# Kernel tuning notes

Measured on AMD Instinct MI355X. Metric: run time of the kernel, lower is better.

Reference implementation:

```python
import jax, jax.numpy as jnp
import numpy as np

N_NODES = 50000
N_EDGES = 800000
F_NODE = 64
F_EDGE = 32
F_GLOBAL = 32
OUT_DIM = 64
N_GRAPHS = 256


def setup_inputs() -> dict:
    key = jax.random.key(0)
    ks = jax.random.split(key, 8)
    x = jax.random.normal(ks[0], (N_NODES, F_NODE), dtype=jnp.float32)
    edge_index = jax.random.randint(ks[1], (2, N_EDGES), 0, N_NODES, dtype=jnp.int64)
    edge_attr = jax.random.normal(ks[2], (N_EDGES, F_EDGE), dtype=jnp.float32)
    u = jax.random.normal(ks[3], (N_GRAPHS, F_GLOBAL), dtype=jnp.float32)
    batch = jnp.sort(jax.random.randint(ks[4], (N_NODES,), 0, N_GRAPHS, dtype=jnp.int64))
    # params (scaled like default Linear init)
    W1 = jax.random.normal(ks[5], (F_NODE + F_EDGE, OUT_DIM), dtype=jnp.float32) / np.sqrt(F_NODE + F_EDGE)
    b1 = jnp.zeros((OUT_DIM,), dtype=jnp.float32)
    W2 = jax.random.normal(ks[6], (F_NODE + OUT_DIM + F_GLOBAL, OUT_DIM), dtype=jnp.float32) / np.sqrt(F_NODE + OUT_DIM + F_GLOBAL)
    b2 = jnp.zeros((OUT_DIM,), dtype=jnp.float32)
    return {"x": x, "edge_index": edge_index, "edge_attr": edge_attr,
            "u": u, "batch": batch, "W1": W1, "b1": b1, "W2": W2, "b2": b2}


def reference(x, edge_index, edge_attr, u, batch, W1, b1, W2, b2):
    dest, src = edge_index[0], edge_index[1]
    # gather source node features + edge attrs -> [E, F_NODE + F_EDGE]
    edge_info = jnp.concatenate([x[src], edge_attr], axis=1)
    # node_mlp_1: Linear + ReLU
    edge_messages = jax.nn.relu(edge_info @ W1 + b1)  # [E, OUT_DIM]
    # scatter-sum into destination nodes
    aggregated = jax.ops.segment_sum(edge_messages, dest, num_segments=x.shape[0])  # [N, OUT_DIM]
    # concat node, aggregated messages, per-graph global
    node_info = jnp.concatenate([x, aggregated, u[batch]], axis=1)  # [N, F_NODE+OUT_DIM+F_GLOBAL]
    # node_mlp_2: Linear + ReLU
    return jax.nn.relu(node_info @ W2 + b2)  # [N, OUT_DIM]
```

## Files before the change

kernel.cpp:

```cpp
#include <hip/hip_runtime.h>
#include <hip/hip_bf16.h>

typedef __attribute__((ext_vector_type(8))) short short8;
typedef __attribute__((ext_vector_type(4))) float f32x4;

constexpr int NN = 50000;
constexpr int NE = 800000;
constexpr int FN = 64;
constexpr int FE = 32;
constexpr int FG = 32;
constexpr int OD = 64;
constexpr int NG = 256;

constexpr int SCAN_B = 256;
constexpr int NBLK = (NN + SCAN_B - 1) / SCAN_B;

constexpr int AGG_BLOCKS = 2048;
constexpr int AGG_WAVES  = AGG_BLOCKS * 4;
constexpr int NWIN       = NN / 16;
constexpr int NODE_BLOCKS = 512;
constexpr int NODE_WAVES  = NODE_BLOCKS * 4;

static __device__ __forceinline__ unsigned pack_bf16(float a, float b) {
    __hip_bfloat162 h = __float22bfloat162_rn(float2{a, b});
    return *reinterpret_cast<unsigned*>(&h);
}

__global__ __launch_bounds__(256) void k_xcvt(const float* __restrict__ x,
                                              unsigned* __restrict__ xb32) {
    const int i = blockIdx.x * 256 + threadIdx.x;
    if (i >= NN * FN / 8) return;
    const float4* p = (const float4*)(x + (size_t)i * 8);
    float4 f0 = p[0], f1 = p[1];
    uint4 o;
    o.x = pack_bf16(f0.x, f0.y);
    o.y = pack_bf16(f0.z, f0.w);
    o.z = pack_bf16(f1.x, f1.y);
    o.w = pack_bf16(f1.z, f1.w);
    ((uint4*)xb32)[i] = o;
}

__global__ __launch_bounds__(256) void k_uw2(const float* __restrict__ u,
                                             const float* __restrict__ W2,
                                             const float* __restrict__ b2,
                                             float* __restrict__ uW2b) {
    const int lane = threadIdx.x & 63;
    float wcol[FG];
#pragma unroll
    for (int k = 0; k < FG; ++k) wcol[k] = W2[(FN + OD + k) * OD + lane];
    const float bias = b2[lane];

    int g = (blockIdx.x * blockDim.x + threadIdx.x) >> 6;
    g = __builtin_amdgcn_readfirstlane(g);
    if (g >= NG) return;

    const float* __restrict__ urow = u + (size_t)g * FG;
    float acc = bias;
#pragma unroll
    for (int k = 0; k < FG; ++k) acc = fmaf(urow[k], wcol[k], acc);
    uW2b[(size_t)g * OD + lane] = acc;
}

__global__ __launch_bounds__(256) void k_hist(const int* __restrict__ ei,
                                              int* __restrict__ cnt) {
    const int e = blockIdx.x * blockDim.x + threadIdx.x;
    if (e < NE) atomicAdd(&cnt[ei[e]], 1);
}

__global__ __launch_bounds__(SCAN_B) void k_scan1(const int* __restrict__ cnt,
                                                  int* __restrict__ start,
                                                  int* __restrict__ bsum) {
    __shared__ int lds[SCAN_B];
    const int i = blockIdx.x * SCAN_B + threadIdx.x;
    const int v = (i < NN) ? cnt[i] : 0;
    lds[threadIdx.x] = v;
    __syncthreads();
#pragma unroll
    for (int off = 1; off < SCAN_B; off <<= 1) {
        int t = (threadIdx.x >= off) ? lds[threadIdx.x - off] : 0;
        __syncthreads();
        lds[threadIdx.x] += t;
        __syncthreads();
    }
    const int incl = lds[threadIdx.x];
    if (i < NN) start[i] = incl - v;
    if (threadIdx.x == SCAN_B - 1) bsum[blockIdx.x] = incl;
}

__global__ __launch_bounds__(SCAN_B) void k_scan2(const int* __restrict__ bsum,
                                                  int* __restrict__ bscan) {
    __shared__ int lds[SCAN_B];
    const int i = threadIdx.x;
    const int v = (i < NBLK) ? bsum[i] : 0;
    lds[i] = v;
    __syncthreads();
#pragma unroll
    for (int off = 1; off < SCAN_B; off <<= 1) {
        int t = (i >= off) ? lds[i - off] : 0;
        __syncthreads();
        lds[i] += t;
        __syncthreads();
    }
    if (i < NBLK) bscan[i] = lds[i] - v;
}

__global__ __launch_bounds__(SCAN_B) void k_scan3(int* __restrict__ start,
                                                  const int* __restrict__ bscan,
                                                  int* __restrict__ cursor) {
    const int i = blockIdx.x * SCAN_B + threadIdx.x;
    if (i < NN) {
        const int s = start[i] + bscan[blockIdx.x];
        start[i] = s;
        cursor[i] = s;
    }
    if (i == 0) start[NN] = NE;
}

__global__ __launch_bounds__(256) void k_scatter(const int* __restrict__ ei,
                                                 int* __restrict__ cursor,
                                                 int2* __restrict__ bucket) {
    const int e = blockIdx.x * blockDim.x + threadIdx.x;
    if (e < NE) {
        const int dst = ei[e];
        const int src = ei[NE + e];
        const int pos = atomicAdd(&cursor[dst], 1);
        bucket[pos] = make_int2(src, e);
    }
}

__global__ __launch_bounds__(256) void k_aggm(const int2* __restrict__ bucket,
                                              const float* __restrict__ ea,
                                              const unsigned short* __restrict__ xb,
                                              const float* __restrict__ W1,
                                              const float* __restrict__ b1,
                                              const int* __restrict__ start,
                                              unsigned short* __restrict__ aggb) {
    const int l = threadIdx.x & 63;
    const int g = l >> 4;
    const int c = l & 15;

    short8 wf[3][4];
#pragma unroll
    for (int t = 0; t < 3; ++t)
#pragma unroll
        for (int b = 0; b < 4; ++b)
#pragma unroll
            for (int i = 0; i < 8; i += 2) {
                const int k = 32 * t + 8 * g + i;
                const unsigned p = pack_bf16(W1[k * OD + (c + 16 * b)],
                                             W1[(k + 1) * OD + (c + 16 * b)]);
                ((unsigned*)&wf[t][b])[i / 2] = p;
            }
    float bias[4];
#pragma unroll
    for (int b = 0; b < 4; ++b) bias[b] = b1[c + 16 * b];

    int wv = (blockIdx.x * blockDim.x + threadIdx.x) >> 6;
    wv = __builtin_amdgcn_readfirstlane(wv);

    for (int n = wv; n < NN; n += AGG_WAVES) {
        const int s0 = start[n];
        const int s1 = start[n + 1];

        f32x4 wsum[4] = {f32x4{0,0,0,0}, f32x4{0,0,0,0},
                         f32x4{0,0,0,0}, f32x4{0,0,0,0}};

        for (int w0 = s0; w0 < s1; w0 += 16) {
            const int valid = s1 - w0;
            int idx = w0 + c;
            if (idx >= s1) idx = s1 - 1;
            const int2 se = bucket[idx];

            short8 a0, a1, a2;
            {
                const uint4* xr = (const uint4*)(xb + (size_t)se.x * FN);
                uint4 q0 = xr[g];
                uint4 q1 = xr[4 + g];
                a0 = *(short8*)&q0;
                a1 = *(short8*)&q1;
            }
            {
                const float4* er = (const float4*)(ea + (size_t)se.y * FE);
                float4 e0 = er[2 * g], e1 = er[2 * g + 1];
                uint4 q2;
                q2.x = pack_bf16(e0.x, e0.y);
                q2.y = pack_bf16(e0.z, e0.w);
                q2.z = pack_bf16(e1.x, e1.y);
                q2.w = pack_bf16(e1.z, e1.w);
                a2 = *(short8*)&q2;
            }

#pragma unroll
            for (int b = 0; b < 4; ++b) {
                f32x4 acc = {0.f, 0.f, 0.f, 0.f};
                acc = __builtin_amdgcn_mfma_f32_16x16x32_bf16(a0, wf[0][b], acc, 0, 0, 0);
                acc = __builtin_amdgcn_mfma_f32_16x16x32_bf16(a1, wf[1][b], acc, 0, 0, 0);
                acc = __builtin_amdgcn_mfma_f32_16x16x32_bf16(a2, wf[2][b], acc, 0, 0, 0);
#pragma unroll
                for (int q = 0; q < 4; ++q) {
                    const int row = g * 4 + q;
                    float v = fmaxf(acc[q] + bias[b], 0.0f);
                    wsum[b][q] += (row < valid) ? v : 0.0f;
                }
            }
        }

        float s0v = wsum[0][0] + wsum[0][1] + wsum[0][2] + wsum[0][3];
        float s1v = wsum[1][0] + wsum[1][1] + wsum[1][2] + wsum[1][3];
        float s2v = wsum[2][0] + wsum[2][1] + wsum[2][2] + wsum[2][3];
        float s3v = wsum[3][0] + wsum[3][1] + wsum[3][2] + wsum[3][3];
        s0v += __shfl_xor(s0v, 16); s0v += __shfl_xor(s0v, 32);
        s1v += __shfl_xor(s1v, 16); s1v += __shfl_xor(s1v, 32);
        s2v += __shfl_xor(s2v, 16); s2v += __shfl_xor(s2v, 32);
        s3v += __shfl_xor(s3v, 16); s3v += __shfl_xor(s3v, 32);

        float v = s0v;
        v = (g == 1) ? s1v : v;
        v = (g == 2) ? s2v : v;
        v = (g == 3) ? s3v : v;
        __hip_bfloat16 hb = __float2bfloat16(v);
        aggb[(size_t)n * OD + c + 16 * g] = *reinterpret_cast<unsigned short*>(&hb);
    }
}

__global__ __launch_bounds__(256) void k_nodem(const unsigned short* __restrict__ xb,
                                               const unsigned short* __restrict__ aggb,
                                               const int* __restrict__ bat,
                                               const float* __restrict__ uW2b,
                                               const float* __restrict__ W2,
                                               float* __restrict__ out) {
    const int l = threadIdx.x & 63;
    const int g = l >> 4;
    const int c = l & 15;

    short8 wf[4][4];
#pragma unroll
    for (int t = 0; t < 4; ++t)
#pragma unroll
        for (int b = 0; b < 4; ++b)
#pragma unroll
            for (int i = 0; i < 8; i += 2) {
                const int k = 32 * t + 8 * g + i;
                const unsigned p = pack_bf16(W2[k * OD + (c + 16 * b)],
                                             W2[(k + 1) * OD + (c + 16 * b)]);
                ((unsigned*)&wf[t][b])[i / 2] = p;
            }

    int wv = (blockIdx.x * blockDim.x + threadIdx.x) >> 6;
    wv = __builtin_amdgcn_readfirstlane(wv);

    for (int w = wv; w < NWIN; w += NODE_WAVES) {
        const int n0 = w * 16;

        const uint4* xr = (const uint4*)(xb + (size_t)(n0 + c) * FN);
        const uint4* ar = (const uint4*)(aggb + (size_t)(n0 + c) * OD);
        uint4 qx0 = xr[g], qx1 = xr[4 + g];
        uint4 qa0 = ar[g], qa1 = ar[4 + g];
        short8 a0 = *(short8*)&qx0, a1 = *(short8*)&qx1;
        short8 a2 = *(short8*)&qa0, a3 = *(short8*)&qa1;

        int bq[4];
#pragma unroll
        for (int q = 0; q < 4; ++q) bq[q] = bat[n0 + g * 4 + q];

#pragma unroll
        for (int b = 0; b < 4; ++b) {
            f32x4 acc = {0.f, 0.f, 0.f, 0.f};
            acc = __builtin_amdgcn_mfma_f32_16x16x32_bf16(a0, wf[0][b], acc, 0, 0, 0);
            acc = __builtin_amdgcn_mfma_f32_16x16x32_bf16(a1, wf[1][b], acc, 0, 0, 0);
            acc = __builtin_amdgcn_mfma_f32_16x16x32_bf16(a2, wf[2][b], acc, 0, 0, 0);
            acc = __builtin_amdgcn_mfma_f32_16x16x32_bf16(a3, wf[3][b], acc, 0, 0, 0);
#pragma unroll
            for (int q = 0; q < 4; ++q) {
                const int n = n0 + g * 4 + q;
                const float val = acc[q] + uW2b[(size_t)bq[q] * OD + c + 16 * b];
                out[(size_t)n * OD + c + 16 * b] = fmaxf(val, 0.0f);
            }
        }
    }
}

extern "C" void kernel_launch(void* const* d_in, const int* in_sizes, int n_in,
                              void* d_out, int out_size, void* d_ws, size_t ws_size,
                              hipStream_t stream) {
    const float* x    = (const float*)d_in[0];
    const int*   ei   = (const int*)d_in[1];
    const float* ea   = (const float*)d_in[2];
    const float* u    = (const float*)d_in[3];
    const int*   bat  = (const int*)d_in[4];
    const float* W1   = (const float*)d_in[5];
    const float* b1   = (const float*)d_in[6];
    const float* W2   = (const float*)d_in[7];
    const float* b2   = (const float*)d_in[8];
    float* out = (float*)d_out;

    char* ws = (char*)d_ws;
    auto alloc = [&](size_t bytes) {
        char* p = ws;
        ws += (bytes + 255) & ~size_t(255);
        return p;
    };
    unsigned short* xb   = (unsigned short*)alloc((size_t)NN * FN * 2);
    unsigned short* aggb = (unsigned short*)alloc((size_t)NN * OD * 2);
    float* uW2b   = (float*)alloc((size_t)NG * OD * sizeof(float));
    int*   cnt    = (int*)alloc((size_t)NN * sizeof(int));
    int*   start  = (int*)alloc((size_t)(NN + 1) * sizeof(int));
    int*   cursor = (int*)alloc((size_t)NN * sizeof(int));
    int*   bsum   = (int*)alloc((size_t)NBLK * sizeof(int));
    int*   bscan  = (int*)alloc((size_t)NBLK * sizeof(int));
    int2*  bucket = (int2*)alloc((size_t)NE * sizeof(int2));

    hipMemsetAsync(cnt, 0, (size_t)NN * sizeof(int), stream);

    k_xcvt<<<dim3((NN * FN / 8 + 255) / 256), dim3(256), 0, stream>>>(x, (unsigned*)xb);
    k_uw2<<<dim3((NG * 64 + 255) / 256), dim3(256), 0, stream>>>(u, W2, b2, uW2b);

    k_hist<<<dim3((NE + 255) / 256), dim3(256), 0, stream>>>(ei, cnt);
    k_scan1<<<dim3(NBLK), dim3(SCAN_B), 0, stream>>>(cnt, start, bsum);
    k_scan2<<<dim3(1), dim3(SCAN_B), 0, stream>>>(bsum, bscan);
    k_scan3<<<dim3(NBLK), dim3(SCAN_B), 0, stream>>>(start, bscan, cursor);
    k_scatter<<<dim3((NE + 255) / 256), dim3(256), 0, stream>>>(ei, cursor, bucket);

    k_aggm<<<dim3(AGG_BLOCKS), dim3(256), 0, stream>>>(bucket, ea, xb, W1, b1, start, aggb);

    k_nodem<<<dim3(NODE_BLOCKS), dim3(256), 0, stream>>>(xb, aggb, bat, uW2b, W2, out);
}
```

Baseline: 169.6 us.

## Pad CSR buckets to 16-edge windows and split aggregation into window and reduce kernels

Each node's edge bucket is padded to a multiple of 16 slots. Pad slots point to a zero row of x and edge 0. The aggregation kernel now processes flat 16-edge windows with no per-node loop or masking and writes per-window partial sums. A new reduction kernel sums the windows for each node and subtracts a precomputed pad correction, relu(ea[0]·W1_e + b1). This balances work across waves when degrees vary, but it adds extra slots, a fill kernel, a partial-sum buffer round trip and one more launch.

```diff
diff --git a/kernel.cpp b/kernel.cpp
--- a/kernel.cpp
+++ b/kernel.cpp
@@ -15,6 +15,7 @@
 constexpr int SCAN_B = 256;
 constexpr int NBLK = (NN + SCAN_B - 1) / SCAN_B;
 
+constexpr int SLOTS_MAX = NE + 15 * NN;
 constexpr int AGG_BLOCKS = 2048;
 constexpr int AGG_WAVES  = AGG_BLOCKS * 4;
 constexpr int NWIN       = NN / 16;
@@ -24,6 +25,19 @@
 static __device__ __forceinline__ unsigned pack_bf16(float a, float b) {
     __hip_bfloat162 h = __float22bfloat162_rn(float2{a, b});
     return *reinterpret_cast<unsigned*>(&h);
+}
+static __device__ __forceinline__ float bf16r(float v) {
+    __hip_bfloat16 h = __float2bfloat16(v);
+    return __bfloat162float(h);
+}
+
+__global__ __launch_bounds__(256) void k_fill(int2* __restrict__ bucket,
+                                              int* __restrict__ cnt,
+                                              unsigned* __restrict__ xb32) {
+    const int i = blockIdx.x * 256 + threadIdx.x;
+    if (i < SLOTS_MAX) bucket[i] = make_int2(NN, 0);
+    if (i < NN) cnt[i] = 0;
+    if (i < 32) xb32[NN * 32 + i] = 0;
 }
 
 __global__ __launch_bounds__(256) void k_xcvt(const float* __restrict__ x,
@@ -40,10 +54,28 @@
     ((uint4*)xb32)[i] = o;
 }
 
-__global__ __launch_bounds__(256) void k_uw2(const float* __restrict__ u,
+__global__ __launch_bounds__(256) void k_pre(const float* __restrict__ u,
                                              const float* __restrict__ W2,
                                              const float* __restrict__ b2,
-                                             float* __restrict__ uW2b) {
+                                             const float* __restrict__ ea,
+                                             const float* __restrict__ W1,
+                                             const float* __restrict__ b1,
+                                             float* __restrict__ uW2b,
+                                             float* __restrict__ corr) {
+    if (blockIdx.x == NG / 4) {
+        const int j = threadIdx.x;
+        if (j < OD) {
+            float acc = b1[j];
+#pragma unroll
+            for (int k = 0; k < FE; ++k) {
+                const float ek = bf16r(ea[k]);
+                const float wk = bf16r(W1[(FN + k) * OD + j]);
+                acc = fmaf(ek, wk, acc);
+            }
+            corr[j] = fmaxf(acc, 0.0f);
+        }
+        return;
+    }
     const int lane = threadIdx.x & 63;
     float wcol[FG];
 #pragma unroll
@@ -68,11 +100,11 @@
 }
 
 __global__ __launch_bounds__(SCAN_B) void k_scan1(const int* __restrict__ cnt,
-                                                  int* __restrict__ start,
+                                                  int* __restrict__ pstart,
                                                   int* __restrict__ bsum) {
     __shared__ int lds[SCAN_B];
     const int i = blockIdx.x * SCAN_B + threadIdx.x;
-    const int v = (i < NN) ? cnt[i] : 0;
+    const int v = (i < NN) ? (((cnt[i] + 15) >> 4) << 4) : 0;
     lds[threadIdx.x] = v;
     __syncthreads();
 #pragma unroll
@@ -83,7 +115,7 @@
         __syncthreads();
     }
     const int incl = lds[threadIdx.x];
-    if (i < NN) start[i] = incl - v;
+    if (i < NN) pstart[i] = incl - v;
     if (threadIdx.x == SCAN_B - 1) bsum[blockIdx.x] = incl;
 }
 
@@ -104,16 +136,17 @@
     if (i < NBLK) bscan[i] = lds[i] - v;
 }
 
-__global__ __launch_bounds__(SCAN_B) void k_scan3(int* __restrict__ start,
+__global__ __launch_bounds__(SCAN_B) void k_scan3(int* __restrict__ pstart,
                                                   const int* __restrict__ bscan,
+                                                  const int* __restrict__ cnt,
                                                   int* __restrict__ cursor) {
     const int i = blockIdx.x * SCAN_B + threadIdx.x;
     if (i < NN) {
-        const int s = start[i] + bscan[blockIdx.x];
-        start[i] = s;
+        const int s = pstart[i] + bscan[blockIdx.x];
+        pstart[i] = s;
         cursor[i] = s;
-    }
-    if (i == 0) start[NN] = NE;
+        if (i == NN - 1) pstart[NN] = s + (((cnt[i] + 15) >> 4) << 4);
+    }
 }
 
 __global__ __launch_bounds__(256) void k_scatter(const int* __restrict__ ei,
@@ -128,13 +161,13 @@
     }
 }
 
-__global__ __launch_bounds__(256) void k_aggm(const int2* __restrict__ bucket,
+__global__ __launch_bounds__(256) void k_aggw(const int2* __restrict__ bucket,
                                               const float* __restrict__ ea,
                                               const unsigned short* __restrict__ xb,
                                               const float* __restrict__ W1,
                                               const float* __restrict__ b1,
-                                              const int* __restrict__ start,
-                                              unsigned short* __restrict__ aggb) {
+                                              const int* __restrict__ pstart,
+                                              float* __restrict__ partial) {
     const int l = threadIdx.x & 63;
     const int g = l >> 4;
     const int c = l & 15;
@@ -155,72 +188,73 @@
 #pragma unroll
     for (int b = 0; b < 4; ++b) bias[b] = b1[c + 16 * b];
 
+    const int nwin = pstart[NN] >> 4;
+
     int wv = (blockIdx.x * blockDim.x + threadIdx.x) >> 6;
     wv = __builtin_amdgcn_readfirstlane(wv);
 
-    for (int n = wv; n < NN; n += AGG_WAVES) {
-        const int s0 = start[n];
-        const int s1 = start[n + 1];
-
-        f32x4 wsum[4] = {f32x4{0,0,0,0}, f32x4{0,0,0,0},
-                         f32x4{0,0,0,0}, f32x4{0,0,0,0}};
-
-        for (int w0 = s0; w0 < s1; w0 += 16) {
-            const int valid = s1 - w0;
-            int idx = w0 + c;
-            if (idx >= s1) idx = s1 - 1;
-            const int2 se = bucket[idx];
-
-            short8 a0, a1, a2;
-            {
-                const uint4* xr = (const uint4*)(xb + (size_t)se.x * FN);
-                uint4 q0 = xr[g];
-                uint4 q1 = xr[4 + g];
-                a0 = *(short8*)&q0;
-                a1 = *(short8*)&q1;
-            }
-            {
-                const float4* er = (const float4*)(ea + (size_t)se.y * FE);
-                float4 e0 = er[2 * g], e1 = er[2 * g + 1];
-                uint4 q2;
-                q2.x = pack_bf16(e0.x, e0.y);
-                q2.y = pack_bf16(e0.z, e0.w);
-                q2.z = pack_bf16(e1.x, e1.y);
-                q2.w = pack_bf16(e1.z, e1.w);
-                a2 = *(short8*)&q2;
-            }
-
-#pragma unroll
-            for (int b = 0; b < 4; ++b) {
-                f32x4 acc = {0.f, 0.f, 0.f, 0.f};
-                acc = __builtin_amdgcn_mfma_f32_16x16x32_bf16(a0, wf[0][b], acc, 0, 0, 0);
-                acc = __builtin_amdgcn_mfma_f32_16x16x32_bf16(a1, wf[1][b], acc, 0, 0, 0);
-                acc = __builtin_amdgcn_mfma_f32_16x16x32_bf16(a2, wf[2][b], acc, 0, 0, 0);
-#pragma unroll
-                for (int q = 0; q < 4; ++q) {
-                    const int row = g * 4 + q;
-                    float v = fmaxf(acc[q] + bias[b], 0.0f);
-                    wsum[b][q] += (row < valid) ? v : 0.0f;
-                }
-            }
-        }
-
-        float s0v = wsum[0][0] + wsum[0][1] + wsum[0][2] + wsum[0][3];
-        float s1v = wsum[1][0] + wsum[1][1] + wsum[1][2] + wsum[1][3];
-        float s2v = wsum[2][0] + wsum[2][1] + wsum[2][2] + wsum[2][3];
-        float s3v = wsum[3][0] + wsum[3][1] + wsum[3][2] + wsum[3][3];
-        s0v += __shfl_xor(s0v, 16); s0v += __shfl_xor(s0v, 32);
-        s1v += __shfl_xor(s1v, 16); s1v += __shfl_xor(s1v, 32);
-        s2v += __shfl_xor(s2v, 16); s2v += __shfl_xor(s2v, 32);
-        s3v += __shfl_xor(s3v, 16); s3v += __shfl_xor(s3v, 32);
-
-        float v = s0v;
-        v = (g == 1) ? s1v : v;
-        v = (g == 2) ? s2v : v;
-        v = (g == 3) ? s3v : v;
-        __hip_bfloat16 hb = __float2bfloat16(v);
-        aggb[(size_t)n * OD + c + 16 * g] = *reinterpret_cast<unsigned short*>(&hb);
-    }
+#pragma unroll 2
+    for (int w = wv; w < nwin; w += AGG_WAVES) {
+        const int2 se = bucket[(size_t)w * 16 + c];
+
+        short8 a0, a1, a2;
+        {
+            const uint4* xr = (const uint4*)(xb + (size_t)se.x * FN);
+            uint4 q0 = xr[g];
+            uint4 q1 = xr[4 + g];
+            a0 = *(short8*)&q0;
+            a1 = *(short8*)&q1;
+        }
+        {
+            const float4* er = (const float4*)(ea + (size_t)se.y * FE);
+            float4 e0 = er[2 * g], e1 = er[2 * g + 1];
+            uint4 q2;
+            q2.x = pack_bf16(e0.x, e0.y);
+            q2.y = pack_bf16(e0.z, e0.w);
+            q2.z = pack_bf16(e1.x, e1.y);
+            q2.w = pack_bf16(e1.z, e1.w);
+            a2 = *(short8*)&q2;
+        }
+
+        float sv[4];
+#pragma unroll
+        for (int b = 0; b < 4; ++b) {
+            f32x4 acc = {0.f, 0.f, 0.f, 0.f};
+            acc = __builtin_amdgcn_mfma_f32_16x16x32_bf16(a0, wf[0][b], acc, 0, 0, 0);
+            acc = __builtin_amdgcn_mfma_f32_16x16x32_bf16(a1, wf[1][b], acc, 0, 0, 0);
+            acc = __builtin_amdgcn_mfma_f32_16x16x32_bf16(a2, wf[2][b], acc, 0, 0, 0);
+            float s = fmaxf(acc[0] + bias[b], 0.0f) + fmaxf(acc[1] + bias[b], 0.0f)
+                    + fmaxf(acc[2] + bias[b], 0.0f) + fmaxf(acc[3] + bias[b], 0.0f);
+            s += __shfl_xor(s, 16);
+            s += __shfl_xor(s, 32);
+            sv[b] = s;
+        }
+        float v = sv[0];
+        v = (g == 1) ? sv[1] : v;
+        v = (g == 2) ? sv[2] : v;
+        v = (g == 3) ? sv[3] : v;
+        partial[(size_t)w * 64 + l] = v;
+    }
+}
+
+__global__ __launch_bounds__(256) void k_red(const float* __restrict__ partial,
+                                             const int* __restrict__ pstart,
+                                             const int* __restrict__ cnt,
+                                             const float* __restrict__ corr,
+                                             unsigned short* __restrict__ aggb) {
+    const int l = threadIdx.x & 63;
+    int n = (blockIdx.x * blockDim.x + threadIdx.x) >> 6;
+    n = __builtin_amdgcn_readfirstlane(n);
+    if (n >= NN) return;
+
+    const int w0 = pstart[n] >> 4;
+    const int w1 = pstart[n + 1] >> 4;
+    float s = 0.0f;
+    for (int w = w0; w < w1; ++w) s += partial[(size_t)w * 64 + l];
+    const int pads = ((w1 - w0) << 4) - cnt[n];
+    s -= (float)pads * corr[l];
+    __hip_bfloat16 hb = __float2bfloat16(s);
+    aggb[(size_t)n * OD + l] = *reinterpret_cast<unsigned short*>(&hb);
 }
 
 __global__ __launch_bounds__(256) void k_nodem(const unsigned short* __restrict__ xb,
@@ -251,7 +285,6 @@
 
     for (int w = wv; w < NWIN; w += NODE_WAVES) {
         const int n0 = w * 16;
-
         const uint4* xr = (const uint4*)(xb + (size_t)(n0 + c) * FN);
         const uint4* ar = (const uint4*)(aggb + (size_t)(n0 + c) * OD);
         uint4 qx0 = xr[g], qx1 = xr[4 + g];
@@ -300,28 +333,31 @@
         ws += (bytes + 255) & ~size_t(255);
         return p;
     };
-    unsigned short* xb   = (unsigned short*)alloc((size_t)NN * FN * 2);
+    unsigned short* xb   = (unsigned short*)alloc((size_t)(NN + 1) * FN * 2);
     unsigned short* aggb = (unsigned short*)alloc((size_t)NN * OD * 2);
-    float* uW2b   = (float*)alloc((size_t)NG * OD * sizeof(float));
-    int*   cnt    = (int*)alloc((size_t)NN * sizeof(int));
-    int*   start  = (int*)alloc((size_t)(NN + 1) * sizeof(int));
-    int*   cursor = (int*)alloc((size_t)NN * sizeof(int));
-    int*   bsum   = (int*)alloc((size_t)NBLK * sizeof(int));
-    int*   bscan  = (int*)alloc((size_t)NBLK * sizeof(int));
-    int2*  bucket = (int2*)alloc((size_t)NE * sizeof(int2));
-
-    hipMemsetAsync(cnt, 0, (size_t)NN * sizeof(int), stream);
+    float* uW2b    = (float*)alloc((size_t)NG * OD * sizeof(float));
+    float* corr    = (float*)alloc((size_t)OD * sizeof(float));
+    int*   cnt     = (int*)alloc((size_t)NN * sizeof(int));
+    int*   pstart  = (int*)alloc((size_t)(NN + 1) * sizeof(int));
+    int*   cursor  = (int*)alloc((size_t)NN * sizeof(int));
+    int*   bsum    = (int*)alloc((size_t)NBLK * sizeof(int));
+    int*   bscan   = (int*)alloc((size_t)NBLK * sizeof(int));
+    int2*  bucket  = (int2*)alloc((size_t)SLOTS_MAX * sizeof(int2));
+    float* partial = (float*)alloc((size_t)(SLOTS_MAX / 16) * OD * sizeof(float));
+
+    k_fill<<<dim3((SLOTS_MAX + 255) / 256), dim3(256), 0, stream>>>(bucket, cnt, (unsigned*)xb);
 
     k_xcvt<<<dim3((NN * FN / 8 + 255) / 256), dim3(256), 0, stream>>>(x, (unsigned*)xb);
-    k_uw2<<<dim3((NG * 64 + 255) / 256), dim3(256), 0, stream>>>(u, W2, b2, uW2b);
+    k_pre<<<dim3(NG / 4 + 1), dim3(256), 0, stream>>>(u, W2, b2, ea, W1, b1, uW2b, corr);
 
     k_hist<<<dim3((NE + 255) / 256), dim3(256), 0, stream>>>(ei, cnt);
-    k_scan1<<<dim3(NBLK), dim3(SCAN_B), 0, stream>>>(cnt, start, bsum);
+    k_scan1<<<dim3(NBLK), dim3(SCAN_B), 0, stream>>>(cnt, pstart, bsum);
     k_scan2<<<dim3(1), dim3(SCAN_B), 0, stream>>>(bsum, bscan);
-    k_scan3<<<dim3(NBLK), dim3(SCAN_B), 0, stream>>>(start, bscan, cursor);
+    k_scan3<<<dim3(NBLK), dim3(SCAN_B), 0, stream>>>(pstart, bscan, cnt, cursor);
     k_scatter<<<dim3((NE + 255) / 256), dim3(256), 0, stream>>>(ei, cursor, bucket);
 
-    k_aggm<<<dim3(AGG_BLOCKS), dim3(256), 0, stream>>>(bucket, ea, xb, W1, b1, start, aggb);
+    k_aggw<<<dim3(AGG_BLOCKS), dim3(256), 0, stream>>>(bucket, ea, xb, W1, b1, pstart, partial);
+    k_red<<<dim3((NN * 64 + 255) / 256), dim3(256), 0, stream>>>(partial, pstart, cnt, corr, aggb);
 
     k_nodem<<<dim3(NODE_BLOCKS), dim3(256), 0, stream>>>(xb, aggb, bat, uW2b, W2, out);
 }
```

Measured after the change: 173.5 us. +2.3%, slower.

## Compute edge messages in edge order and scatter, then segment-reduce per node

Applied to the files above, without the earlier changes.

Replaces the bucket-then-gather design with a per-edge kernel. It computes each 16-edge window's messages with MFMA in natural edge order, takes a slot through an atomic cursor, and writes the fp16 message rows into a destination-sorted buffer. A separate kernel then sums each node's contiguous message rows. This removes the random edge_attr gathers and the padding waste from partially filled per-node windows. In exchange it writes and re-reads a large E x 64 fp16 intermediate and stores messages at reduced precision. The node kernel block count is also retuned.

```diff
diff --git a/kernel.cpp b/kernel.cpp
--- a/kernel.cpp
+++ b/kernel.cpp
@@ -1,5 +1,6 @@
 #include <hip/hip_runtime.h>
 #include <hip/hip_bf16.h>
+#include <hip/hip_fp16.h>
 
 typedef __attribute__((ext_vector_type(8))) short short8;
 typedef __attribute__((ext_vector_type(4))) float f32x4;
@@ -15,10 +16,11 @@
 constexpr int SCAN_B = 256;
 constexpr int NBLK = (NN + SCAN_B - 1) / SCAN_B;
 
-constexpr int AGG_BLOCKS = 2048;
-constexpr int AGG_WAVES  = AGG_BLOCKS * 4;
-constexpr int NWIN       = NN / 16;
-constexpr int NODE_BLOCKS = 512;
+constexpr int NWIN_E = NE / 16;
+constexpr int MS_BLOCKS = 2048;
+constexpr int MS_WAVES  = MS_BLOCKS * 4;
+constexpr int NWIN_N = NN / 16;
+constexpr int NODE_BLOCKS = 782;
 constexpr int NODE_WAVES  = NODE_BLOCKS * 4;
 
 static __device__ __forceinline__ unsigned pack_bf16(float a, float b) {
@@ -106,35 +108,24 @@
 
 __global__ __launch_bounds__(SCAN_B) void k_scan3(int* __restrict__ start,
                                                   const int* __restrict__ bscan,
+                                                  const int* __restrict__ cnt,
                                                   int* __restrict__ cursor) {
     const int i = blockIdx.x * SCAN_B + threadIdx.x;
     if (i < NN) {
         const int s = start[i] + bscan[blockIdx.x];
         start[i] = s;
         cursor[i] = s;
-    }
-    if (i == 0) start[NN] = NE;
-}
-
-__global__ __launch_bounds__(256) void k_scatter(const int* __restrict__ ei,
+        if (i == NN - 1) start[NN] = s + cnt[i];
+    }
+}
+
+__global__ __launch_bounds__(256) void k_msgscat(const int* __restrict__ ei,
+                                                 const float* __restrict__ ea,
+                                                 const unsigned short* __restrict__ xb,
+                                                 const float* __restrict__ W1,
+                                                 const float* __restrict__ b1,
                                                  int* __restrict__ cursor,
-                                                 int2* __restrict__ bucket) {
-    const int e = blockIdx.x * blockDim.x + threadIdx.x;
-    if (e < NE) {
-        const int dst = ei[e];
-        const int src = ei[NE + e];
-        const int pos = atomicAdd(&cursor[dst], 1);
-        bucket[pos] = make_int2(src, e);
-    }
-}
-
-__global__ __launch_bounds__(256) void k_aggm(const int2* __restrict__ bucket,
-                                              const float* __restrict__ ea,
-                                              const unsigned short* __restrict__ xb,
-                                              const float* __restrict__ W1,
-                                              const float* __restrict__ b1,
-                                              const int* __restrict__ start,
-                                              unsigned short* __restrict__ aggb) {
+                                                 unsigned short* __restrict__ mbuf) {
     const int l = threadIdx.x & 63;
     const int g = l >> 4;
     const int c = l & 15;
@@ -158,69 +149,85 @@
     int wv = (blockIdx.x * blockDim.x + threadIdx.x) >> 6;
     wv = __builtin_amdgcn_readfirstlane(wv);
 
-    for (int n = wv; n < NN; n += AGG_WAVES) {
-        const int s0 = start[n];
-        const int s1 = start[n + 1];
-
-        f32x4 wsum[4] = {f32x4{0,0,0,0}, f32x4{0,0,0,0},
-                         f32x4{0,0,0,0}, f32x4{0,0,0,0}};
-
-        for (int w0 = s0; w0 < s1; w0 += 16) {
-            const int valid = s1 - w0;
-            int idx = w0 + c;
-            if (idx >= s1) idx = s1 - 1;
-            const int2 se = bucket[idx];
-
-            short8 a0, a1, a2;
-            {
-                const uint4* xr = (const uint4*)(xb + (size_t)se.x * FN);
-                uint4 q0 = xr[g];
-                uint4 q1 = xr[4 + g];
-                a0 = *(short8*)&q0;
-                a1 = *(short8*)&q1;
-            }
-            {
-                const float4* er = (const float4*)(ea + (size_t)se.y * FE);
-                float4 e0 = er[2 * g], e1 = er[2 * g + 1];
-                uint4 q2;
-                q2.x = pack_bf16(e0.x, e0.y);
-                q2.y = pack_bf16(e0.z, e0.w);
-                q2.z = pack_bf16(e1.x, e1.y);
-                q2.w = pack_bf16(e1.z, e1.w);
-                a2 = *(short8*)&q2;
-            }
-
-#pragma unroll
-            for (int b = 0; b < 4; ++b) {
-                f32x4 acc = {0.f, 0.f, 0.f, 0.f};
-                acc = __builtin_amdgcn_mfma_f32_16x16x32_bf16(a0, wf[0][b], acc, 0, 0, 0);
-                acc = __builtin_amdgcn_mfma_f32_16x16x32_bf16(a1, wf[1][b], acc, 0, 0, 0);
-                acc = __builtin_amdgcn_mfma_f32_16x16x32_bf16(a2, wf[2][b], acc, 0, 0, 0);
-#pragma unroll
-                for (int q = 0; q < 4; ++q) {
-                    const int row = g * 4 + q;
-                    float v = fmaxf(acc[q] + bias[b], 0.0f);
-                    wsum[b][q] += (row < valid) ? v : 0.0f;
-                }
-            }
-        }
-
-        float s0v = wsum[0][0] + wsum[0][1] + wsum[0][2] + wsum[0][3];
-        float s1v = wsum[1][0] + wsum[1][1] + wsum[1][2] + wsum[1][3];
-        float s2v = wsum[2][0] + wsum[2][1] + wsum[2][2] + wsum[2][3];
-        float s3v = wsum[3][0] + wsum[3][1] + wsum[3][2] + wsum[3][3];
-        s0v += __shfl_xor(s0v, 16); s0v += __shfl_xor(s0v, 32);
-        s1v += __shfl_xor(s1v, 16); s1v += __shfl_xor(s1v, 32);
-        s2v += __shfl_xor(s2v, 16); s2v += __shfl_xor(s2v, 32);
-        s3v += __shfl_xor(s3v, 16); s3v += __shfl_xor(s3v, 32);
-
-        float v = s0v;
-        v = (g == 1) ? s1v : v;
-        v = (g == 2) ? s2v : v;
-        v = (g == 3) ? s3v : v;
-        __hip_bfloat16 hb = __float2bfloat16(v);
-        aggb[(size_t)n * OD + c + 16 * g] = *reinterpret_cast<unsigned short*>(&hb);
-    }
+    for (int w = wv; w < NWIN_E; w += MS_WAVES) {
+        const int e = w * 16 + c;
+        const int dst = ei[e];
+        const int src = ei[NE + e];
+        int pos = 0;
+        if (l < 16) pos = atomicAdd(&cursor[dst], 1);
+
+        short8 a0, a1, a2;
+        {
+            const uint4* xr = (const uint4*)(xb + (size_t)src * FN);
+            uint4 q0 = xr[g];
+            uint4 q1 = xr[4 + g];
+            a0 = *(short8*)&q0;
+            a1 = *(short8*)&q1;
+        }
+        {
+            const float4* er = (const float4*)(ea + (size_t)e * FE);
+            float4 e0 = er[2 * g], e1 = er[2 * g + 1];
+            uint4 q2;
+            q2.x = pack_bf16(e0.x, e0.y);
+            q2.y = pack_bf16(e0.z, e0.w);
+            q2.z = pack_bf16(e1.x, e1.y);
+            q2.w = pack_bf16(e1.z, e1.w);
+            a2 = *(short8*)&q2;
+        }
+
+        f32x4 accb[4];
+#pragma unroll
+        for (int b = 0; b < 4; ++b) {
+            f32x4 acc = {0.f, 0.f, 0.f, 0.f};
+            acc = __builtin_amdgcn_mfma_f32_16x16x32_bf16(a0, wf[0][b], acc, 0, 0, 0);
+            acc = __builtin_amdgcn_mfma_f32_16x16x32_bf16(a1, wf[1][b], acc, 0, 0, 0);
+            acc = __builtin_amdgcn_mfma_f32_16x16x32_bf16(a2, wf[2][b], acc, 0, 0, 0);
+            accb[b] = acc;
+        }
+
+#pragma unroll
+        for (int q = 0; q < 4; ++q) {
+            const int pr = __shfl(pos, 4 * g + q);
+            const float v0 = fmaxf(accb[0][q] + bias[0], 0.0f);
+            const float v1 = fmaxf(accb[1][q] + bias[1], 0.0f);
+            const float v2 = fmaxf(accb[2][q] + bias[2], 0.0f);
+            const float v3 = fmaxf(accb[3][q] + bias[3], 0.0f);
+            const __half2 h01 = __float22half2_rn(float2{v0, v1});
+            const __half2 h23 = __float22half2_rn(float2{v2, v3});
+            uint2 out;
+            out.x = *reinterpret_cast<const unsigned*>(&h01);
+            out.y = *reinterpret_cast<const unsigned*>(&h23);
+            *reinterpret_cast<uint2*>(mbuf + (size_t)pr * 64 + c * 4) = out;
+        }
+    }
+}
+
+__global__ __launch_bounds__(256) void k_segred(const unsigned short* __restrict__ mbuf,
+                                                const int* __restrict__ start,
+                                                unsigned short* __restrict__ aggb) {
+    const int l = threadIdx.x & 63;
+    int n = (blockIdx.x * blockDim.x + threadIdx.x) >> 6;
+    n = __builtin_amdgcn_readfirstlane(n);
+    if (n >= NN) return;
+
+    const int r0 = start[n];
+    const int r1 = start[n + 1];
+    const __half* mh = (const __half*)mbuf;
+
+    float s0 = 0.0f, s1 = 0.0f, s2 = 0.0f, s3 = 0.0f;
+    int r = r0;
+    for (; r + 3 < r1; r += 4) {
+        s0 += __half2float(mh[(size_t)(r + 0) * 64 + l]);
+        s1 += __half2float(mh[(size_t)(r + 1) * 64 + l]);
+        s2 += __half2float(mh[(size_t)(r + 2) * 64 + l]);
+        s3 += __half2float(mh[(size_t)(r + 3) * 64 + l]);
+    }
+    for (; r < r1; ++r) s0 += __half2float(mh[(size_t)r * 64 + l]);
+    const float s = (s0 + s1) + (s2 + s3);
+
+    const int tc = (l >> 2) + 16 * (l & 3);
+    __hip_bfloat16 hb = __float2bfloat16(s);
+    aggb[(size_t)n * OD + tc] = *reinterpret_cast<unsigned short*>(&hb);
 }
 
 __global__ __launch_bounds__(256) void k_nodem(const unsigned short* __restrict__ xb,
@@ -249,9 +256,8 @@
     int wv = (blockIdx.x * blockDim.x + threadIdx.x) >> 6;
     wv = __builtin_amdgcn_readfirstlane(wv);
 
-    for (int w = wv; w < NWIN; w += NODE_WAVES) {
+    for (int w = wv; w < NWIN_N; w += NODE_WAVES) {
         const int n0 = w * 16;
-
         const uint4* xr = (const uint4*)(xb + (size_t)(n0 + c) * FN);
         const uint4* ar = (const uint4*)(aggb + (size_t)(n0 + c) * OD);
         uint4 qx0 = xr[g], qx1 = xr[4 + g];
@@ -302,13 +308,13 @@
     };
     unsigned short* xb   = (unsigned short*)alloc((size_t)NN * FN * 2);
     unsigned short* aggb = (unsigned short*)alloc((size_t)NN * OD * 2);
-    float* uW2b   = (float*)alloc((size_t)NG * OD * sizeof(float));
-    int*   cnt    = (int*)alloc((size_t)NN * sizeof(int));
-    int*   start  = (int*)alloc((size_t)(NN + 1) * sizeof(int));
-    int*   cursor = (int*)alloc((size_t)NN * sizeof(int));
-    int*   bsum   = (int*)alloc((size_t)NBLK * sizeof(int));
-    int*   bscan  = (int*)alloc((size_t)NBLK * sizeof(int));
-    int2*  bucket = (int2*)alloc((size_t)NE * sizeof(int2));
+    float* uW2b    = (float*)alloc((size_t)NG * OD * sizeof(float));
+    int*   cnt     = (int*)alloc((size_t)NN * sizeof(int));
+    int*   start   = (int*)alloc((size_t)(NN + 1) * sizeof(int));
+    int*   cursor  = (int*)alloc((size_t)NN * sizeof(int));
+    int*   bsum    = (int*)alloc((size_t)NBLK * sizeof(int));
+    int*   bscan   = (int*)alloc((size_t)NBLK * sizeof(int));
+    unsigned short* mbuf = (unsigned short*)alloc((size_t)NE * OD * 2);
 
     hipMemsetAsync(cnt, 0, (size_t)NN * sizeof(int), stream);
 
@@ -318,10 +324,11 @@
     k_hist<<<dim3((NE + 255) / 256), dim3(256), 0, stream>>>(ei, cnt);
     k_scan1<<<dim3(NBLK), dim3(SCAN_B), 0, stream>>>(cnt, start, bsum);
     k_scan2<<<dim3(1), dim3(SCAN_B), 0, stream>>>(bsum, bscan);
-    k_scan3<<<dim3(NBLK), dim3(SCAN_B), 0, stream>>>(start, bscan, cursor);
-    k_scatter<<<dim3((NE + 255) / 256), dim3(256), 0, stream>>>(ei, cursor, bucket);
-
-    k_aggm<<<dim3(AGG_BLOCKS), dim3(256), 0, stream>>>(bucket, ea, xb, W1, b1, start, aggb);
+    k_scan3<<<dim3(NBLK), dim3(SCAN_B), 0, stream>>>(start, bscan, cnt, cursor);
+
+    k_msgscat<<<dim3(MS_BLOCKS), dim3(256), 0, stream>>>(ei, ea, xb, W1, b1, cursor, mbuf);
+
+    k_segred<<<dim3((NN * 64 + 255) / 256), dim3(256), 0, stream>>>(mbuf, start, aggb);
 
     k_nodem<<<dim3(NODE_BLOCKS), dim3(256), 0, stream>>>(xb, aggb, bat, uW2b, W2, out);
 }
```

After: 154.6 us. -8.8%, faster.
